# Optimization experiments

Hardware: AMD Instinct MI355X
Metric: run time of the kernel (lower is better)

## Reference

```python
import jax, jax.numpy as jnp
import numpy as np

M, N, F = 512, 128, 512  # molecules, atoms per molecule, feature dim
HID, OUT = F // 4, 1


def setup_inputs() -> dict:
    key = jax.random.key(0)
    k1, k2, k3 = jax.random.split(key, 3)
    h = jax.random.normal(k1, (M, N, F), dtype=jnp.float32)
    W1 = jax.random.normal(k2, (F, HID), dtype=jnp.float32) * (1.0 / np.sqrt(F))
    b1 = jnp.zeros((HID,), dtype=jnp.float32)
    W2 = jax.random.normal(k3, (HID, OUT), dtype=jnp.float32) * (1.0 / np.sqrt(HID))
    b2 = jnp.zeros((OUT,), dtype=jnp.float32)
    return {"h": h, "W1": W1, "b1": b1, "W2": W2, "b2": b2}


def reference(h, W1, b1, W2, b2):
    # method == 'weighted_summation'
    # gate MLP: Linear -> ReLU -> Linear -> Sigmoid, per atom
    w = jax.nn.sigmoid(jax.nn.relu(h @ W1 + b1) @ W2 + b2)  # [M, N, OUT]
    # per-molecule weighted sum over atoms: mm(w_h.T, h) for each molecule,
    # concatenated along dim 0 -> [M*OUT, F] (OUT=1 -> [M, F])
    out = jnp.einsum('mno,mnf->mof', w, h)  # [M, OUT, F]
    return out.reshape(M * OUT, F)
```

## Files before the change

kernel.cpp:

```cpp
#include <hip/hip_runtime.h>
#include <hip/hip_bf16.h>


typedef unsigned short u16;
typedef unsigned int u32;
typedef __bf16 bf16x8 __attribute__((ext_vector_type(8)));
typedef float f32x4 __attribute__((ext_vector_type(4)));
typedef float f32x2 __attribute__((ext_vector_type(2)));
typedef u32 u32x4 __attribute__((ext_vector_type(4)));

#define M_MOL 512
#define F_DIM 512
#define HID_DIM 128
#define ABLK 32
#define NBLK (M_MOL * 4)

static __device__ __forceinline__ u16 f2bf(float x) {
  u32 u = __float_as_uint(x);
  u32 r = (u + 0x7fffu + ((u >> 16) & 1u)) >> 16;
  return (u16)r;
}
static __device__ __forceinline__ bf16x8 pack8(u32x4 a, u32x4 b) {
  u32x4 r;
  r[0] = (a[0] >> 16) | (a[1] & 0xffff0000u);
  r[1] = (a[2] >> 16) | (a[3] & 0xffff0000u);
  r[2] = (b[0] >> 16) | (b[1] & 0xffff0000u);
  r[3] = (b[2] >> 16) | (b[3] & 0xffff0000u);
  return __builtin_bit_cast(bf16x8, r);
}

__global__ __launch_bounds__(256) void transpose_w1(const float* __restrict__ W1,
                                                    u16* __restrict__ W1Tt) {
  __shared__ float tile[64][65];
  const int k0 = blockIdx.x * 64;
  const int n0 = blockIdx.y * 64;
  const int t = threadIdx.x;
  #pragma unroll
  for (int i = 0; i < 16; ++i) {
    const int lin = i * 256 + t;
    const int lr = lin >> 6, lc = lin & 63;
    tile[lc][lr] = W1[(size_t)(k0 + lr) * HID_DIM + (n0 + lc)];
  }
  __syncthreads();
  #pragma unroll
  for (int i = 0; i < 16; ++i) {
    const int lin = i * 256 + t;
    const int wr = lin >> 6, wc = lin & 63;
    const int k = k0 + wc;
    const int hid = n0 + wr;
    W1Tt[(size_t)(((k >> 5) * 4 + ((k >> 3) & 3)) * HID_DIM + hid) * 8 + (k & 7)] =
        f2bf(tile[wr][wc]);
  }
}

__global__ __launch_bounds__(256, 3) void pool_partial(
    const float* __restrict__ h, const u16* __restrict__ W1Tt,
    const float* __restrict__ b1, const float* __restrict__ W2,
    const float* __restrict__ b2, float* __restrict__ part) {
  __shared__ u16 As[ABLK * F_DIM];
  __shared__ u16 bt[2][4096];
  __shared__ float wred[2][ABLK];
  __shared__ float w_s[ABLK];

  const int blk = blockIdx.x;
  const int tid = threadIdx.x;
  const int wv = tid >> 6;
  const int lane = tid & 63;
  const int quad = lane >> 4;
  const int cl = lane & 15;
  const int strip = wv >> 1;
  const int hh = wv & 1;

  const u16* gB = W1Tt + wv * 1024 + lane * 8;
  #define DMA_TILE(ks, buf)                                                        \
    do {                                                                           \
      const u16* _g = gB + (size_t)(ks) * 4096;                                    \
      u16* _l = &bt[buf][wv * 1024];                                               \
      __builtin_amdgcn_global_load_lds(                                            \
          (const __attribute__((address_space(1))) u32*)(const void*)_g,           \
          (__attribute__((address_space(3))) u32*)(void*)_l, 16, 0, 0);            \
      __builtin_amdgcn_global_load_lds(                                            \
          (const __attribute__((address_space(1))) u32*)(const void*)(_g + 512),   \
          (__attribute__((address_space(3))) u32*)(void*)(_l + 512), 16, 0, 0);    \
    } while (0)

  DMA_TILE(0, 0);

  {
    const u32x4* hg = (const u32x4*)(h + (size_t)blk * ABLK * F_DIM);
    u32x4 L[8], H[8];
    #pragma unroll
    for (int i = 0; i < 8; ++i) {
      const int u = i * 256 + tid;
      L[i] = hg[2 * u];
      H[i] = hg[2 * u + 1];
    }
    #pragma unroll
    for (int i = 0; i < 8; ++i) {
      const int u = i * 256 + tid;
      const int row = u >> 6, c = u & 63;
      const int phys = (c & ~7) | ((c ^ row) & 7);
      *(bf16x8*)(As + row * F_DIM + phys * 8) = pack8(L[i], H[i]);
    }
  }
  __syncthreads();

  f32x4 acc[4];
  #pragma unroll
  for (int t = 0; t < 4; ++t) acc[t] = (f32x4){0.f, 0.f, 0.f, 0.f};

  const int ar = strip * 16 + cl;
  const u16* aBase = As + ar * F_DIM;

  for (int ks = 0; ks < 16; ++ks) {
    if (ks < 15) DMA_TILE(ks + 1, (ks + 1) & 1);
    const int c = ks * 4 + quad;
    const int aphys = (c & ~7) | ((c ^ ar) & 7);
    bf16x8 afr = *(const bf16x8*)(aBase + aphys * 8);
    const u16* bb = bt[ks & 1] + quad * (HID_DIM * 8);
    #pragma unroll
    for (int t = 0; t < 4; ++t) {
      bf16x8 bfr = *(const bf16x8*)(bb + ((hh * 4 + t) * 16 + cl) * 8);
      acc[t] = __builtin_amdgcn_mfma_f32_16x16x32_bf16(afr, bfr, acc[t], 0, 0, 0);
    }
    if (ks < 15) __syncthreads();
  }

  float psum[4] = {0.f, 0.f, 0.f, 0.f};
  #pragma unroll
  for (int t = 0; t < 4; ++t) {
    const int hid = (hh * 4 + t) * 16 + cl;
    const float b1v = b1[hid];
    const float w2v = W2[hid];
    #pragma unroll
    for (int r = 0; r < 4; ++r) {
      float tv = fmaxf(acc[t][r] + b1v, 0.f);
      psum[r] = fmaf(tv, w2v, psum[r]);
    }
  }
  #pragma unroll
  for (int off = 1; off < 16; off <<= 1)
    #pragma unroll
    for (int r = 0; r < 4; ++r)
      psum[r] += __shfl_xor(psum[r], off, 64);
  if (cl == 0) {
    #pragma unroll
    for (int r = 0; r < 4; ++r)
      wred[hh][strip * 16 + quad * 4 + r] = psum[r];
  }
  __syncthreads();
  if (tid < ABLK)
    w_s[tid] = 1.f / (1.f + __expf(-(wred[0][tid] + wred[1][tid] + b2[0])));
  __syncthreads();

  float facc[8] = {0.f, 0.f, 0.f, 0.f, 0.f, 0.f, 0.f, 0.f};
  #pragma unroll
  for (int i = 0; i < 8; ++i) {
    const int row = wv * 8 + i;
    const float wn = w_s[row];
    const int phys = (lane & ~7) | ((lane ^ row) & 7);
    bf16x8 hv = *(const bf16x8*)(As + row * F_DIM + phys * 8);
    u32x4 uv = __builtin_bit_cast(u32x4, hv);
    #pragma unroll
    for (int j = 0; j < 4; ++j) {
      facc[2 * j]     = fmaf(wn, __uint_as_float(uv[j] << 16), facc[2 * j]);
      facc[2 * j + 1] = fmaf(wn, __uint_as_float(uv[j] & 0xffff0000u), facc[2 * j + 1]);
    }
  }
  float (*red)[F_DIM] = (float (*)[F_DIM])bt;
  #pragma unroll
  for (int j = 0; j < 8; ++j) red[wv][lane * 8 + j] = facc[j];
  __syncthreads();

  {
    const int f = tid * 2;
    f32x2 o;
    o[0] = red[0][f] + red[1][f] + red[2][f] + red[3][f];
    o[1] = red[0][f + 1] + red[1][f + 1] + red[2][f + 1] + red[3][f + 1];
    *(f32x2*)(part + (size_t)blk * F_DIM + f) = o;
  }
}

__global__ __launch_bounds__(256) void reduce_out(const float* __restrict__ part,
                                                  float* __restrict__ out) {
  const int m = blockIdx.x;
  const int f = threadIdx.x * 2;
  f32x2 o = (f32x2){0.f, 0.f};
  #pragma unroll
  for (int p = 0; p < 4; ++p) {
    f32x2 a = *(const f32x2*)(part + (size_t)(4 * m + p) * F_DIM + f);
    o[0] += a[0];
    o[1] += a[1];
  }
  *(f32x2*)(out + (size_t)m * F_DIM + f) = o;
}

extern "C" void kernel_launch(void* const* d_in, const int* in_sizes, int n_in,
                              void* d_out, int out_size, void* d_ws, size_t ws_size,
                              hipStream_t stream) {
  const float* h  = (const float*)d_in[0];
  const float* W1 = (const float*)d_in[1];
  const float* b1 = (const float*)d_in[2];
  const float* W2 = (const float*)d_in[3];
  const float* b2 = (const float*)d_in[4];
  float* out = (float*)d_out;

  u16* W1Tt = (u16*)d_ws;
  float* part = (float*)((char*)d_ws + (size_t)HID_DIM * F_DIM * sizeof(u16));

  transpose_w1<<<dim3(8, 2), 256, 0, stream>>>(W1, W1Tt);
  pool_partial<<<NBLK, 256, 0, stream>>>(h, W1Tt, b1, W2, b2, part);
  reduce_out<<<M_MOL, 256, 0, stream>>>(part, out);
}
```

Measured before the change: 218.4 us.

## Use 2-wave blocks with direct global W1 fragment loads and atomic output reduction

Shrinks pool_partial blocks from four waves to two, so each wave computes all 128 hidden units for its own 16 atoms. W1 fragments are now read straight from global memory (L2-resident) rather than staged in LDS with double-buffered DMA, which removes the per-k-step barriers and the cross-wave gate reduction. The separate reduce_out kernel is replaced by a zero_out kernel followed by float atomic adds into the output. The trade-offs are fewer waves per block, more global/L2 traffic for W1, and atomics whose summation order is not deterministic.

Measured after the change: 220.5 us. About the same (+1.0%).

```diff
diff --git a/kernel.cpp b/kernel.cpp
--- a/kernel.cpp
+++ b/kernel.cpp
@@ -6,7 +6,6 @@
 typedef unsigned int u32;
 typedef __bf16 bf16x8 __attribute__((ext_vector_type(8)));
 typedef float f32x4 __attribute__((ext_vector_type(4)));
-typedef float f32x2 __attribute__((ext_vector_type(2)));
 typedef u32 u32x4 __attribute__((ext_vector_type(4)));
 
 #define M_MOL 512
@@ -53,13 +52,16 @@
   }
 }
 
-__global__ __launch_bounds__(256, 3) void pool_partial(
+__global__ __launch_bounds__(256) void zero_out(float* __restrict__ out) {
+  ((f32x4*)out)[blockIdx.x * 256 + threadIdx.x] = (f32x4){0.f, 0.f, 0.f, 0.f};
+}
+
+__global__ __launch_bounds__(128, 2) void pool_partial(
     const float* __restrict__ h, const u16* __restrict__ W1Tt,
     const float* __restrict__ b1, const float* __restrict__ W2,
-    const float* __restrict__ b2, float* __restrict__ part) {
+    const float* __restrict__ b2, float* __restrict__ out) {
   __shared__ u16 As[ABLK * F_DIM];
-  __shared__ u16 bt[2][4096];
-  __shared__ float wred[2][ABLK];
+  __shared__ float red[2][F_DIM];
   __shared__ float w_s[ABLK];
 
   const int blk = blockIdx.x;
@@ -68,68 +70,53 @@
   const int lane = tid & 63;
   const int quad = lane >> 4;
   const int cl = lane & 15;
-  const int strip = wv >> 1;
-  const int hh = wv & 1;
-
-  const u16* gB = W1Tt + wv * 1024 + lane * 8;
-  #define DMA_TILE(ks, buf)                                                        \
-    do {                                                                           \
-      const u16* _g = gB + (size_t)(ks) * 4096;                                    \
-      u16* _l = &bt[buf][wv * 1024];                                               \
-      __builtin_amdgcn_global_load_lds(                                            \
-          (const __attribute__((address_space(1))) u32*)(const void*)_g,           \
-          (__attribute__((address_space(3))) u32*)(void*)_l, 16, 0, 0);            \
-      __builtin_amdgcn_global_load_lds(                                            \
-          (const __attribute__((address_space(1))) u32*)(const void*)(_g + 512),   \
-          (__attribute__((address_space(3))) u32*)(void*)(_l + 512), 16, 0, 0);    \
-    } while (0)
-
-  DMA_TILE(0, 0);
 
   {
     const u32x4* hg = (const u32x4*)(h + (size_t)blk * ABLK * F_DIM);
-    u32x4 L[8], H[8];
     #pragma unroll
-    for (int i = 0; i < 8; ++i) {
-      const int u = i * 256 + tid;
-      L[i] = hg[2 * u];
-      H[i] = hg[2 * u + 1];
-    }
-    #pragma unroll
-    for (int i = 0; i < 8; ++i) {
-      const int u = i * 256 + tid;
-      const int row = u >> 6, c = u & 63;
-      const int phys = (c & ~7) | ((c ^ row) & 7);
-      *(bf16x8*)(As + row * F_DIM + phys * 8) = pack8(L[i], H[i]);
+    for (int half = 0; half < 2; ++half) {
+      u32x4 L[8], H[8];
+      #pragma unroll
+      for (int i = 0; i < 8; ++i) {
+        const int u = (half * 8 + i) * 128 + tid;
+        L[i] = hg[2 * u];
+        H[i] = hg[2 * u + 1];
+      }
+      #pragma unroll
+      for (int i = 0; i < 8; ++i) {
+        const int u = (half * 8 + i) * 128 + tid;
+        const int row = u >> 6, c = u & 63;
+        const int phys = (c & ~7) | ((c ^ row) & 7);
+        *(bf16x8*)(As + row * F_DIM + phys * 8) = pack8(L[i], H[i]);
+      }
     }
   }
   __syncthreads();
 
-  f32x4 acc[4];
+  f32x4 acc[8];
   #pragma unroll
-  for (int t = 0; t < 4; ++t) acc[t] = (f32x4){0.f, 0.f, 0.f, 0.f};
+  for (int t = 0; t < 8; ++t) acc[t] = (f32x4){0.f, 0.f, 0.f, 0.f};
 
-  const int ar = strip * 16 + cl;
+  const int ar = wv * 16 + cl;
   const u16* aBase = As + ar * F_DIM;
+  const u16* gB = W1Tt + (quad * HID_DIM + cl) * 8;
 
   for (int ks = 0; ks < 16; ++ks) {
-    if (ks < 15) DMA_TILE(ks + 1, (ks + 1) & 1);
     const int c = ks * 4 + quad;
     const int aphys = (c & ~7) | ((c ^ ar) & 7);
     bf16x8 afr = *(const bf16x8*)(aBase + aphys * 8);
-    const u16* bb = bt[ks & 1] + quad * (HID_DIM * 8);
+    const u16* gk = gB + ks * 4096;
     #pragma unroll
-    for (int t = 0; t < 4; ++t) {
-      bf16x8 bfr = *(const bf16x8*)(bb + ((hh * 4 + t) * 16 + cl) * 8);
+    for (int t = 0; t < 8; ++t) {
+      bf16x8 bfr = *(const bf16x8*)(gk + t * 128);
       acc[t] = __builtin_amdgcn_mfma_f32_16x16x32_bf16(afr, bfr, acc[t], 0, 0, 0);
     }
-    if (ks < 15) __syncthreads();
   }
 
   float psum[4] = {0.f, 0.f, 0.f, 0.f};
   #pragma unroll
-  for (int t = 0; t < 4; ++t) {
-    const int hid = (hh * 4 + t) * 16 + cl;
+  for (int t = 0; t < 8; ++t) {
+    const int hid = t * 16 + cl;
     const float b1v = b1[hid];
     const float w2v = W2[hid];
     #pragma unroll
@@ -144,19 +131,17 @@
     for (int r = 0; r < 4; ++r)
       psum[r] += __shfl_xor(psum[r], off, 64);
   if (cl == 0) {
+    const float b2v = b2[0];
     #pragma unroll
     for (int r = 0; r < 4; ++r)
-      wred[hh][strip * 16 + quad * 4 + r] = psum[r];
+      w_s[wv * 16 + quad * 4 + r] = 1.f / (1.f + __expf(-(psum[r] + b2v)));
   }
-  __syncthreads();
-  if (tid < ABLK)
-    w_s[tid] = 1.f / (1.f + __expf(-(wred[0][tid] + wred[1][tid] + b2[0])));
   __syncthreads();
 
   float facc[8] = {0.f, 0.f, 0.f, 0.f, 0.f, 0.f, 0.f, 0.f};
   #pragma unroll
-  for (int i = 0; i < 8; ++i) {
-    const int row = wv * 8 + i;
+  for (int i = 0; i < 16; ++i) {
+    const int row = wv * 16 + i;
     const float wn = w_s[row];
     const int phys = (lane & ~7) | ((lane ^ row) & 7);
     bf16x8 hv = *(const bf16x8*)(As + row * F_DIM + phys * 8);
@@ -167,32 +152,19 @@
       facc[2 * j + 1] = fmaf(wn, __uint_as_float(uv[j] & 0xffff0000u), facc[2 * j + 1]);
     }
   }
-  float (*red)[F_DIM] = (float (*)[F_DIM])bt;
   #pragma unroll
   for (int j = 0; j < 8; ++j) red[wv][lane * 8 + j] = facc[j];
   __syncthreads();
 
   {
-    const int f = tid * 2;
-    f32x2 o;
-    o[0] = red[0][f] + red[1][f] + red[2][f] + red[3][f];
-    o[1] = red[0][f + 1] + red[1][f + 1] + red[2][f + 1] + red[3][f + 1];
-    *(f32x2*)(part + (size_t)blk * F_DIM + f) = o;
+    const int m = blk >> 2;
+    const int f = tid * 4;
+    #pragma unroll
+    for (int j = 0; j < 4; ++j) {
+      const float o = red[0][f + j] + red[1][f + j];
+      unsafeAtomicAdd(out + (size_t)m * F_DIM + f + j, o);
+    }
   }
-}
-
-__global__ __launch_bounds__(256) void reduce_out(const float* __restrict__ part,
-                                                  float* __restrict__ out) {
-  const int m = blockIdx.x;
-  const int f = threadIdx.x * 2;
-  f32x2 o = (f32x2){0.f, 0.f};
-  #pragma unroll
-  for (int p = 0; p < 4; ++p) {
-    f32x2 a = *(const f32x2*)(part + (size_t)(4 * m + p) * F_DIM + f);
-    o[0] += a[0];
-    o[1] += a[1];
-  }
-  *(f32x2*)(out + (size_t)m * F_DIM + f) = o;
 }
 
 extern "C" void kernel_launch(void* const* d_in, const int* in_sizes, int n_in,
@@ -206,9 +178,8 @@
   float* out = (float*)d_out;
 
   u16* W1Tt = (u16*)d_ws;
-  float* part = (float*)((char*)d_ws + (size_t)HID_DIM * F_DIM * sizeof(u16));
 
   transpose_w1<<<dim3(8, 2), 256, 0, stream>>>(W1, W1Tt);
-  pool_partial<<<NBLK, 256, 0, stream>>>(h, W1Tt, b1, W2, b2, part);
-  reduce_out<<<M_MOL, 256, 0, stream>>>(part, out);
+  zero_out<<<256, 256, 0, stream>>>(out);
+  pool_partial<<<NBLK, 128, 0, stream>>>(h, W1Tt, b1, W2, b2, out);
 }
```
